# Kernel tuning notes

Hardware: AMD Instinct MI355X
Metric: run time of the kernel (lower is better)

The kernel has to match this reference:

```python
import jax, jax.numpy as jnp
import numpy as np

E = 1024      # embed_dim
H = 16        # n_heads
B = 8         # number of varlen segments
LQ = 512      # query tokens per segment (uniform packing)
LKV = 1024    # kv tokens per segment (uniform packing)


def setup_inputs() -> dict:
    key = jax.random.key(0)
    k0, k1, k2, k3 = jax.random.split(key, 4)
    inputs = jax.random.normal(k0, (B * LKV, E), dtype=jnp.float32)
    queries = jax.random.normal(k1, (B * LQ, E), dtype=jnp.float32)
    # cu_seqlens: prefix sums of segment lengths (uniform segments here)
    cu_seqlens_inputs = jnp.arange(B + 1, dtype=jnp.int32) * LKV
    cu_seqlens_queries = jnp.arange(B + 1, dtype=jnp.int32) * LQ
    # nn.MultiheadAttention parameters
    scale = 0.02
    w_in = jax.random.normal(k2, (3 * E, E), dtype=jnp.float32) * scale
    b_in = jnp.zeros((3 * E,), dtype=jnp.float32)
    w_out = jax.random.normal(k3, (E, E), dtype=jnp.float32) * scale
    b_out = jnp.zeros((E,), dtype=jnp.float32)
    return {
        "inputs": inputs,
        "queries": queries,
        "w_in": w_in,
        "b_in": b_in,
        "w_out": w_out,
        "b_out": b_out,
        "cu_seqlens_inputs": cu_seqlens_inputs,
        "cu_seqlens_queries": cu_seqlens_queries,
    }


def reference(inputs, queries, w_in, b_in, w_out, b_out,
              cu_seqlens_inputs, cu_seqlens_queries):
    # Packed varlen cross-attention. Segments are uniform (as produced by
    # setup_inputs), so the ragged computation is expressed as a single
    # batched attention: reshape packed tokens to [B, L, E]. Attention is
    # confined within each segment, matching the original per-segment loop.
    e = inputs.shape[-1]
    dh = e // H
    b = cu_seqlens_inputs.shape[0] - 1
    lkv = inputs.shape[0] // b
    lq = queries.shape[0] // b

    # in_proj: torch computes x @ W.T + b with W = in_proj_weight rows [q;k;v]
    q = queries @ w_in[:e].T + b_in[:e]
    k = inputs @ w_in[e:2 * e].T + b_in[e:2 * e]
    v = inputs @ w_in[2 * e:].T + b_in[2 * e:]

    q = q.reshape(b, lq, H, dh)
    k = k.reshape(b, lkv, H, dh)
    v = v.reshape(b, lkv, H, dh)

    scale = 1.0 / jnp.sqrt(jnp.asarray(dh, q.dtype))
    scores = jnp.einsum('bqhd,bkhd->bhqk', q, k) * scale   # [B,H,Lq,Lkv]
    probs = jax.nn.softmax(scores, axis=-1)
    o = jnp.einsum('bhqk,bkhd->bqhd', probs, v).reshape(b * lq, e)
    return o @ w_out.T + b_out
```

## Files before the change

### kernel.cpp

```cpp
#include <hip/hip_runtime.h>

#define E_DIM 1024
#define NH 16
#define DH 64
#define BSEG 8
#define LQ 512
#define LKV 1024

typedef short bf16x8 __attribute__((ext_vector_type(8)));
typedef float f32x4 __attribute__((ext_vector_type(4)));
typedef unsigned short u16;

__device__ __forceinline__ u16 f2bf(float x) {
    unsigned u = __float_as_uint(x);
    u += 0x7FFF + ((u >> 16) & 1);
    return (u16)(u >> 16);
}

__device__ __forceinline__ void async16(const void* g, const void* l) {
    __builtin_amdgcn_global_load_lds(
        (const __attribute__((address_space(1))) unsigned int*)g,
        (__attribute__((address_space(3))) unsigned int*)l, 16, 0, 0);
}

__global__ __launch_bounds__(256) void cvt_all_kernel(
    const float* __restrict__ inputs, const float* __restrict__ queries,
    const float* __restrict__ w_in, const float* __restrict__ w_out,
    u16* __restrict__ ib, u16* __restrict__ qb,
    u16* __restrict__ wib, u16* __restrict__ wob)
{
    int blk = blockIdx.x;
    const float* s; u16* d; int base;
    if (blk < 8192)        { s = inputs;  d = ib;  base = blk; }
    else if (blk < 12288)  { s = queries; d = qb;  base = blk - 8192; }
    else if (blk < 15360)  { s = w_in;    d = wib; base = blk - 12288; }
    else                   { s = w_out;   d = wob; base = blk - 15360; }
    int i = base * 256 + threadIdx.x;
    float4 v = ((const float4*)s)[i];
    ushort4 o;
    o.x = f2bf(v.x); o.y = f2bf(v.y); o.z = f2bf(v.z); o.w = f2bf(v.w);
    ((ushort4*)d)[i] = o;
}

__global__ __launch_bounds__(256) void proj_gemm_kernel(
    const u16* __restrict__ inputs_b, const u16* __restrict__ queries_b,
    const u16* __restrict__ w_in_b, const float* __restrict__ b_in,
    u16* __restrict__ Kf, u16* __restrict__ Qf, u16* __restrict__ Vf)
{
    __shared__ u16 As[128 * 32];
    __shared__ u16 Ws[128 * 32];

    const int bx = blockIdx.x;
    const int by = blockIdx.y;
    const bool isQ = (by >= 64);
    if (isQ && bx >= 8) return;

    const u16* A = isQ ? queries_b : inputs_b;
    const u16* W = w_in_b + (isQ ? 0 : (size_t)E_DIM * E_DIM);
    const float* bias = b_in + (isQ ? 0 : E_DIM);
    const int m_blk = (isQ ? by - 64 : by) * 128;
    const int n_blk = bx * 128;
    const int K = E_DIM;

    const int tid = threadIdx.x;
    const int l = tid & 63;
    const int w = tid >> 6;
    const int m0 = (w & 1) * 64;
    const int n0 = (w >> 1) * 64;
    const int quad = l >> 4;
    const int c = l & 15;

    f32x4 acc[4][4];
    #pragma unroll
    for (int i = 0; i < 4; ++i)
        #pragma unroll
        for (int j = 0; j < 4; ++j)
            acc[i][j] = (f32x4){0.f, 0.f, 0.f, 0.f};

    const int srow = l >> 2;
    const int skoff = (l & 3) * 8;
    const u16* Ag1 = A + (size_t)(m_blk + w * 16 + srow) * K + skoff;
    const u16* Ag2 = A + (size_t)(m_blk + (w + 4) * 16 + srow) * K + skoff;
    const u16* Wg1 = W + (size_t)(n_blk + w * 16 + srow) * K + skoff;
    const u16* Wg2 = W + (size_t)(n_blk + (w + 4) * 16 + srow) * K + skoff;

    for (int k0 = 0; k0 < K; k0 += 32) {
        __syncthreads();
        async16(Ag1 + k0, As + (size_t)w * 512);
        async16(Ag2 + k0, As + (size_t)(w + 4) * 512);
        async16(Wg1 + k0, Ws + (size_t)w * 512);
        async16(Wg2 + k0, Ws + (size_t)(w + 4) * 512);
        __syncthreads();

        bf16x8 af[4], wf[4];
        #pragma unroll
        for (int t = 0; t < 4; ++t) {
            af[t] = *(const bf16x8*)&As[(m0 + t * 16 + c) * 32 + quad * 8];
            wf[t] = *(const bf16x8*)&Ws[(n0 + t * 16 + c) * 32 + quad * 8];
        }
        #pragma unroll
        for (int i = 0; i < 4; ++i)
            #pragma unroll
            for (int j = 0; j < 4; ++j)
                acc[i][j] = __builtin_amdgcn_mfma_f32_16x16x32_bf16(
                    af[i], wf[j], acc[i][j], 0, 0, 0);
    }

    #pragma unroll
    for (int jj = 0; jj < 4; ++jj) {
        int col = n_blk + n0 + jj * 16 + c;
        float bv = bias[col];
        if (isQ || col < 1024) {
            u16* dst = isQ ? Qf : Kf;
            int hh = col >> 6, d = col & 63;
            int dq = d >> 3, dj = d & 7;
            #pragma unroll
            for (int i = 0; i < 4; ++i) {
                int t = (m_blk + m0 + i * 16) >> 4;
                size_t base = ((size_t)(t * NH + hh)) * 1024
                            + (size_t)(dq * 16 + quad * 4) * 8 + dj;
                #pragma unroll
                for (int r = 0; r < 4; ++r)
                    dst[base + (size_t)r * 8] = f2bf(acc[i][jj][r] + bv);
            }
        } else {
            int vcol = col - 1024;
            int hv = vcol >> 6, d = vcol & 63;
            int td = d >> 4, ct = d & 15;
            #pragma unroll
            for (int i = 0; i < 4; ++i) {
                int tok = m_blk + m0 + i * 16;
                int g32 = tok >> 5;
                int jo = (tok & 16) >> 2;
                ushort4 pk;
                pk.x = f2bf(acc[i][jj][0] + bv);
                pk.y = f2bf(acc[i][jj][1] + bv);
                pk.z = f2bf(acc[i][jj][2] + bv);
                pk.w = f2bf(acc[i][jj][3] + bv);
                *(ushort4*)(Vf + ((size_t)(g32 * NH + hv)) * 2048
                            + (size_t)((td * 4 + quad) * 16 + ct) * 8 + jo) = pk;
            }
        }
    }
}

struct KVfrags { bf16x8 kf[4][2]; bf16x8 vf[2][4]; };

__global__ __launch_bounds__(256) void attn_kernel(
    const u16* __restrict__ Qf, const u16* __restrict__ Kf,
    const u16* __restrict__ Vf, u16* __restrict__ Ob)
{
    const int tid = threadIdx.x;
    const int l = tid & 63;
    const int w = tid >> 6;
    const int quad = l >> 4;
    const int c = l & 15;
    const int bid = blockIdx.x;
    const int h = bid & 15;
    const int b = (bid >> 4) & 7;
    const int qt = bid >> 7;
    const int q0 = b * LQ + qt * 64 + w * 16;
    const float C1 = 0.18033688011112042f;

    bf16x8 qf[2];
    {
        size_t qb = ((size_t)((q0 >> 4) * NH + h)) * 1024 + (size_t)l * 8;
        qf[0] = *(const bf16x8*)(Qf + qb);
        qf[1] = *(const bf16x8*)(Qf + qb + 512);
    }

    f32x4 o[4];
    #pragma unroll
    for (int td = 0; td < 4; ++td) o[td] = (f32x4){0.f, 0.f, 0.f, 0.f};
    float m_i = -1e30f, l_i = 0.f;

    auto load_kv = [&](int kv0, KVfrags& dst) {
        const int kvg = b * LKV + kv0;
        #pragma unroll
        for (int nt = 0; nt < 4; ++nt) {
            size_t kb = ((size_t)((((kvg >> 4) + nt) * NH) + h)) * 1024 + (size_t)l * 8;
            dst.kf[nt][0] = *(const bf16x8*)(Kf + kb);
            dst.kf[nt][1] = *(const bf16x8*)(Kf + kb + 512);
        }
        #pragma unroll
        for (int g = 0; g < 2; ++g) {
            size_t vb = ((size_t)((((kvg >> 5) + g) * NH) + h)) * 2048 + (size_t)l * 8;
            #pragma unroll
            for (int td = 0; td < 4; ++td)
                dst.vf[g][td] = *(const bf16x8*)(Vf + vb + td * 512);
        }
    };

    auto step = [&](KVfrags& cv) {
        f32x4 s[4];
        #pragma unroll
        for (int nt = 0; nt < 4; ++nt) s[nt] = (f32x4){0.f, 0.f, 0.f, 0.f};
        #pragma unroll
        for (int nt = 0; nt < 4; ++nt)
            #pragma unroll
            for (int hk = 0; hk < 2; ++hk)
                s[nt] = __builtin_amdgcn_mfma_f32_16x16x32_bf16(
                    cv.kf[nt][hk], qf[hk], s[nt], 0, 0, 0);

        float vm = -1e30f;
        #pragma unroll
        for (int nt = 0; nt < 4; ++nt)
            #pragma unroll
            for (int r = 0; r < 4; ++r) vm = fmaxf(vm, s[nt][r]);
        vm = fmaxf(vm, __shfl_xor(vm, 16, 64));
        vm = fmaxf(vm, __shfl_xor(vm, 32, 64));
        float mnew = fmaxf(m_i, vm);
        float alpha = __builtin_amdgcn_exp2f((m_i - mnew) * C1);
        m_i = mnew;

        float p[4][4];
        float rs = 0.f;
        #pragma unroll
        for (int nt = 0; nt < 4; ++nt)
            #pragma unroll
            for (int r = 0; r < 4; ++r) {
                p[nt][r] = __builtin_amdgcn_exp2f((s[nt][r] - mnew) * C1);
                rs += p[nt][r];
            }
        rs += __shfl_xor(rs, 16, 64);
        rs += __shfl_xor(rs, 32, 64);
        l_i = l_i * alpha + rs;

        float ar[4];
        #pragma unroll
        for (int r = 0; r < 4; ++r) ar[r] = __shfl(alpha, quad * 4 + r, 16);
        #pragma unroll
        for (int td = 0; td < 4; ++td)
            #pragma unroll
            for (int r = 0; r < 4; ++r) o[td][r] *= ar[r];

        bf16x8 af[2];
        #pragma unroll
        for (int g = 0; g < 2; ++g)
            #pragma unroll
            for (int r = 0; r < 4; ++r) {
                af[g][r]     = (short)f2bf(p[2 * g][r]);
                af[g][4 + r] = (short)f2bf(p[2 * g + 1][r]);
            }

        #pragma unroll
        for (int g = 0; g < 2; ++g)
            #pragma unroll
            for (int td = 0; td < 4; ++td)
                o[td] = __builtin_amdgcn_mfma_f32_16x16x32_bf16(
                    af[g], cv.vf[g][td], o[td], 0, 0, 0);
    };

    KVfrags bufA, bufB;
    load_kv(0, bufA);
    #pragma unroll
    for (int it = 0; it < 16; it += 2) {
        if (it + 1 < 16) load_kv((it + 1) * 64, bufB);
        step(bufA);
        if (it + 2 < 16) load_kv((it + 2) * 64, bufA);
        if (it + 1 < 16) step(bufB);
    }

    float invl = 1.f / l_i;
    float ir[4];
    #pragma unroll
    for (int r = 0; r < 4; ++r) ir[r] = __shfl(invl, quad * 4 + r, 16);
    #pragma unroll
    for (int td = 0; td < 4; ++td)
        #pragma unroll
        for (int r = 0; r < 4; ++r)
            Ob[(size_t)(q0 + quad * 4 + r) * E_DIM + h * 64 + td * 16 + c] =
                f2bf(o[td][r] * ir[r]);
}

__global__ __launch_bounds__(256) void out_gemm_kernel(
    const u16* __restrict__ A, const u16* __restrict__ W,
    const float* __restrict__ bias, float* __restrict__ Cf)
{
    __shared__ u16 As[128 * 32];
    __shared__ u16 Ws[128 * 32];

    const int K = E_DIM, N = E_DIM;
    const int tid = threadIdx.x;
    const int l = tid & 63;
    const int w = tid >> 6;
    const int m_blk = blockIdx.y * 128;
    const int n_blk = blockIdx.x * 128;
    const int m0 = (w & 1) * 64;
    const int n0 = (w >> 1) * 64;
    const int quad = l >> 4;
    const int c = l & 15;

    f32x4 acc[4][4];
    #pragma unroll
    for (int i = 0; i < 4; ++i)
        #pragma unroll
        for (int j = 0; j < 4; ++j)
            acc[i][j] = (f32x4){0.f, 0.f, 0.f, 0.f};

    const int srow = l >> 2;
    const int skoff = (l & 3) * 8;
    const u16* Ag1 = A + (size_t)(m_blk + w * 16 + srow) * K + skoff;
    const u16* Ag2 = A + (size_t)(m_blk + (w + 4) * 16 + srow) * K + skoff;
    const u16* Wg1 = W + (size_t)(n_blk + w * 16 + srow) * K + skoff;
    const u16* Wg2 = W + (size_t)(n_blk + (w + 4) * 16 + srow) * K + skoff;

    for (int k0 = 0; k0 < K; k0 += 32) {
        __syncthreads();
        async16(Ag1 + k0, As + (size_t)w * 512);
        async16(Ag2 + k0, As + (size_t)(w + 4) * 512);
        async16(Wg1 + k0, Ws + (size_t)w * 512);
        async16(Wg2 + k0, Ws + (size_t)(w + 4) * 512);
        __syncthreads();

        bf16x8 af[4], wf[4];
        #pragma unroll
        for (int t = 0; t < 4; ++t) {
            af[t] = *(const bf16x8*)&As[(m0 + t * 16 + c) * 32 + quad * 8];
            wf[t] = *(const bf16x8*)&Ws[(n0 + t * 16 + c) * 32 + quad * 8];
        }
        #pragma unroll
        for (int i = 0; i < 4; ++i)
            #pragma unroll
            for (int j = 0; j < 4; ++j)
                acc[i][j] = __builtin_amdgcn_mfma_f32_16x16x32_bf16(
                    af[i], wf[j], acc[i][j], 0, 0, 0);
    }

    #pragma unroll
    for (int j = 0; j < 4; ++j) {
        int col = n_blk + n0 + j * 16 + c;
        float bv = bias[col];
        #pragma unroll
        for (int i = 0; i < 4; ++i) {
            int row = m_blk + m0 + i * 16 + quad * 4;
            #pragma unroll
            for (int r = 0; r < 4; ++r)
                Cf[(size_t)(row + r) * N + col] = acc[i][j][r] + bv;
        }
    }
}

extern "C" void kernel_launch(void* const* d_in, const int* in_sizes, int n_in,
                              void* d_out, int out_size, void* d_ws, size_t ws_size,
                              hipStream_t stream) {
    const float* inputs  = (const float*)d_in[0];
    const float* queries = (const float*)d_in[1];
    const float* w_in    = (const float*)d_in[2];
    const float* b_in    = (const float*)d_in[3];
    const float* w_out   = (const float*)d_in[4];
    const float* b_out   = (const float*)d_in[5];
    float* out = (float*)d_out;

    const int NQ = BSEG * LQ;
    const int NKV = BSEG * LKV;

    u16* inputs_b  = (u16*)d_ws;
    u16* queries_b = inputs_b  + (size_t)NKV * E_DIM;
    u16* w_in_b    = queries_b + (size_t)NQ * E_DIM;
    u16* w_out_b   = w_in_b    + (size_t)3 * E_DIM * E_DIM;
    u16* Qf        = w_out_b   + (size_t)E_DIM * E_DIM;
    u16* Kf        = Qf        + (size_t)NQ * E_DIM;
    u16* Vf        = Kf        + (size_t)NKV * E_DIM;
    u16* Ob        = Vf        + (size_t)NKV * E_DIM;

    dim3 blk(256);

    cvt_all_kernel<<<16384, blk, 0, stream>>>(
        inputs, queries, w_in, w_out, inputs_b, queries_b, w_in_b, w_out_b);

    proj_gemm_kernel<<<dim3(16, 96), blk, 0, stream>>>(
        inputs_b, queries_b, w_in_b, b_in, Kf, Qf, Vf);

    attn_kernel<<<1024, blk, 0, stream>>>(Qf, Kf, Vf, Ob);

    out_gemm_kernel<<<dim3(E_DIM / 128, NQ / 128), blk, 0, stream>>>(
        Ob, w_out_b, b_out, out);
}
```

Baseline: 249.1 us.

## Widen projection GEMM tile to 128x256 and swizzle block order for XCD locality

The projection GEMM tile grows from 128x128 to 128x256, so each warp computes 64x128 with 32 accumulators. This doubles weight reuse per A load and removes the grid of idle early-exit blocks by using a flat 640-block launch. Both GEMMs also remap block indices so consecutive hardware-dispatched blocks (bid&7, likely one per XCD) share rows of A, aiming for better L2 reuse. The cost is higher register pressure and fewer blocks, which may reduce occupancy.

```diff
diff --git a/kernel.cpp b/kernel.cpp
--- a/kernel.cpp
+++ b/kernel.cpp
@@ -48,66 +48,73 @@
     u16* __restrict__ Kf, u16* __restrict__ Qf, u16* __restrict__ Vf)
 {
     __shared__ u16 As[128 * 32];
-    __shared__ u16 Ws[128 * 32];
-
-    const int bx = blockIdx.x;
-    const int by = blockIdx.y;
-    const bool isQ = (by >= 64);
-    if (isQ && bx >= 8) return;
+    __shared__ u16 Ws[256 * 32];
+
+    const int bid = blockIdx.x;
+    const bool isQ = (bid >= 512);
+    const int x = bid & 7;
+    int bx, by;
+    if (!isQ) { int i = bid >> 3;         bx = i >> 3; by = x * 8 + (i & 7); }
+    else      { int i = (bid - 512) >> 3; bx = i >> 2; by = x * 4 + (i & 3); }
 
     const u16* A = isQ ? queries_b : inputs_b;
     const u16* W = w_in_b + (isQ ? 0 : (size_t)E_DIM * E_DIM);
     const float* bias = b_in + (isQ ? 0 : E_DIM);
-    const int m_blk = (isQ ? by - 64 : by) * 128;
-    const int n_blk = bx * 128;
+    const int m_blk = by * 128;
+    const int n_blk = bx * 256;
     const int K = E_DIM;
 
     const int tid = threadIdx.x;
     const int l = tid & 63;
     const int w = tid >> 6;
     const int m0 = (w & 1) * 64;
-    const int n0 = (w >> 1) * 64;
+    const int n0 = (w >> 1) * 128;
     const int quad = l >> 4;
     const int c = l & 15;
 
-    f32x4 acc[4][4];
+    f32x4 acc[4][8];
     #pragma unroll
     for (int i = 0; i < 4; ++i)
         #pragma unroll
-        for (int j = 0; j < 4; ++j)
+        for (int j = 0; j < 8; ++j)
             acc[i][j] = (f32x4){0.f, 0.f, 0.f, 0.f};
 
     const int srow = l >> 2;
     const int skoff = (l & 3) * 8;
-    const u16* Ag1 = A + (size_t)(m_blk + w * 16 + srow) * K + skoff;
-    const u16* Ag2 = A + (size_t)(m_blk + (w + 4) * 16 + srow) * K + skoff;
-    const u16* Wg1 = W + (size_t)(n_blk + w * 16 + srow) * K + skoff;
-    const u16* Wg2 = W + (size_t)(n_blk + (w + 4) * 16 + srow) * K + skoff;
+    const u16* AgA = A + (size_t)(m_blk + w * 16 + srow) * K + skoff;
+    const u16* AgB = A + (size_t)(m_blk + (w + 4) * 16 + srow) * K + skoff;
+    const u16* Wg0 = W + (size_t)(n_blk + w * 16 + srow) * K + skoff;
+    const u16* Wg1 = W + (size_t)(n_blk + (w + 4) * 16 + srow) * K + skoff;
+    const u16* Wg2 = W + (size_t)(n_blk + (w + 8) * 16 + srow) * K + skoff;
+    const u16* Wg3 = W + (size_t)(n_blk + (w + 12) * 16 + srow) * K + skoff;
 
     for (int k0 = 0; k0 < K; k0 += 32) {
         __syncthreads();
-        async16(Ag1 + k0, As + (size_t)w * 512);
-        async16(Ag2 + k0, As + (size_t)(w + 4) * 512);
-        async16(Wg1 + k0, Ws + (size_t)w * 512);
-        async16(Wg2 + k0, Ws + (size_t)(w + 4) * 512);
+        async16(AgA + k0, As + (size_t)w * 512);
+        async16(AgB + k0, As + (size_t)(w + 4) * 512);
+        async16(Wg0 + k0, Ws + (size_t)w * 512);
+        async16(Wg1 + k0, Ws + (size_t)(w + 4) * 512);
+        async16(Wg2 + k0, Ws + (size_t)(w + 8) * 512);
+        async16(Wg3 + k0, Ws + (size_t)(w + 12) * 512);
         __syncthreads();
 
-        bf16x8 af[4], wf[4];
-        #pragma unroll
-        for (int t = 0; t < 4; ++t) {
-            af[t] = *(const bf16x8*)&As[(m0 + t * 16 + c) * 32 + quad * 8];
-            wf[t] = *(const bf16x8*)&Ws[(n0 + t * 16 + c) * 32 + quad * 8];
-        }
+        bf16x8 af[4], wf[8];
+        #pragma unroll
+        for (int t = 0; t < 4; ++t)
+            af[t] = *(const bf16x8*)&As[((m0 >> 4) + t) * 512 + c * 32 + quad * 8];
+        #pragma unroll
+        for (int t = 0; t < 8; ++t)
+            wf[t] = *(const bf16x8*)&Ws[((n0 >> 4) + t) * 512 + c * 32 + quad * 8];
         #pragma unroll
         for (int i = 0; i < 4; ++i)
             #pragma unroll
-            for (int j = 0; j < 4; ++j)
+            for (int j = 0; j < 8; ++j)
                 acc[i][j] = __builtin_amdgcn_mfma_f32_16x16x32_bf16(
                     af[i], wf[j], acc[i][j], 0, 0, 0);
     }
 
     #pragma unroll
-    for (int jj = 0; jj < 4; ++jj) {
+    for (int jj = 0; jj < 8; ++jj) {
         int col = n_blk + n0 + jj * 16 + c;
         float bv = bias[col];
         if (isQ || col < 1024) {
@@ -281,11 +288,15 @@
     __shared__ u16 Ws[128 * 32];
 
     const int K = E_DIM, N = E_DIM;
+    const int bid = blockIdx.x;
+    const int x = bid & 7;
+    const int i_ = bid >> 3;
+    const int m_blk = (x * 4 + (i_ & 3)) * 128;
+    const int n_blk = (i_ >> 2) * 128;
+
     const int tid = threadIdx.x;
     const int l = tid & 63;
     const int w = tid >> 6;
-    const int m_blk = blockIdx.y * 128;
-    const int n_blk = blockIdx.x * 128;
     const int m0 = (w & 1) * 64;
     const int n0 = (w >> 1) * 64;
     const int quad = l >> 4;
@@ -369,11 +380,11 @@
     cvt_all_kernel<<<16384, blk, 0, stream>>>(
         inputs, queries, w_in, w_out, inputs_b, queries_b, w_in_b, w_out_b);
 
-    proj_gemm_kernel<<<dim3(16, 96), blk, 0, stream>>>(
+    proj_gemm_kernel<<<640, blk, 0, stream>>>(
         inputs_b, queries_b, w_in_b, b_in, Kf, Qf, Vf);
 
     attn_kernel<<<1024, blk, 0, stream>>>(Qf, Kf, Vf, Ob);
 
-    out_gemm_kernel<<<dim3(E_DIM / 128, NQ / 128), blk, 0, stream>>>(
+    out_gemm_kernel<<<256, blk, 0, stream>>>(
         Ob, w_out_b, b_out, out);
 }
```

Result: slower. 280.8 us (+12.7%).
